# Performance work log

Measured on AMD Instinct MI355X. Metric: run time of the kernel, lower is better.

Reference implementation:

```python
import jax, jax.numpy as jnp
import numpy as np

SEQ_LEN, INPUT_DIM, HIDDEN_DIM, OUTPUT_DIM = 1024, 128, 256, 128
BATCH = 256


def setup_inputs() -> dict:
    key = jax.random.key(0)
    ks = jax.random.split(key, 7)
    s_ih = 1.0 / np.sqrt(INPUT_DIM)
    s_hh = 1.0 / np.sqrt(HIDDEN_DIM)
    return {
        "x": jax.random.normal(ks[0], (BATCH, SEQ_LEN, INPUT_DIM), jnp.float32),
        "W_ih": jax.random.normal(ks[1], (INPUT_DIM, 4 * HIDDEN_DIM), jnp.float32) * s_ih,
        "W_hh": jax.random.normal(ks[2], (HIDDEN_DIM, 4 * HIDDEN_DIM), jnp.float32) * s_hh,
        "b_ih": jax.random.normal(ks[3], (4 * HIDDEN_DIM,), jnp.float32) * s_hh,
        "b_hh": jax.random.normal(ks[4], (4 * HIDDEN_DIM,), jnp.float32) * s_hh,
        "W_out": jax.random.normal(ks[5], (HIDDEN_DIM, OUTPUT_DIM), jnp.float32) * s_hh,
        "b_out": jax.random.normal(ks[6], (OUTPUT_DIM,), jnp.float32) * s_hh,
    }


def reference(x, W_ih, W_hh, b_ih, b_hh, W_out, b_out):
    B, T, _ = x.shape
    H = W_hh.shape[0]
    # Precompute input projections for all timesteps: [T, B, 4H]
    x_proj = jnp.einsum("bti,ig->tbg", x, W_ih) + (b_ih + b_hh)

    def step(carry, xp_t):
        h, c = carry
        gates = xp_t + h @ W_hh  # [B, 4H]
        i_t, f_t, g_t, o_t = jnp.split(gates, 4, axis=1)
        i_t = jax.nn.sigmoid(i_t)
        f_t = jax.nn.sigmoid(f_t)
        g_t = jnp.tanh(g_t)
        o_t = jax.nn.sigmoid(o_t)
        c = f_t * c + i_t * g_t
        h = o_t * jnp.tanh(c)
        return (h, c), None

    h0 = jnp.zeros((B, H), x.dtype)
    c0 = jnp.zeros((B, H), x.dtype)
    (h_T, _), _ = jax.lax.scan(step, (h0, c0), x_proj)
    return h_T @ W_out + b_out
```

## Files before the change

### kernel.cpp

```cpp
#include <hip/hip_runtime.h>
#include <cstdint>


#define T_    1024
#define I_    128
#define H_    256

typedef short s8v __attribute__((ext_vector_type(8)));
typedef float f4v __attribute__((ext_vector_type(4)));
typedef unsigned short u16;
typedef unsigned int   u32;
typedef unsigned long long u64;

__device__ __forceinline__ u16 f2bf(float f) {
  union { float f; u32 u; } v; v.f = f;
  u32 r = v.u + 0x7FFFu + ((v.u >> 16) & 1u);
  return (u16)(r >> 16);
}
__device__ __forceinline__ float bf2f(u16 h) {
  union { u32 u; float f; } v; v.u = ((u32)h) << 16;
  return v.f;
}
__device__ __forceinline__ float sig_(float x)  { return 1.0f / (1.0f + __expf(-x)); }
__device__ __forceinline__ float tanh_(float x) { return 2.0f / (1.0f + __expf(-2.0f * x)) - 1.0f; }

__device__ __forceinline__ void unpack8(const u64 w[4], s8v& hi, s8v& lo) {
  #pragma unroll
  for (int j = 0; j < 4; j++) {
    u32 a = (u32)w[j], b = (u32)(w[j] >> 32);
    hi[2*j]   = (short)(u16)a;        lo[2*j]   = (short)(u16)(a >> 16);
    hi[2*j+1] = (short)(u16)b;        lo[2*j+1] = (short)(u16)(b >> 16);
  }
}

__global__ __launch_bounds__(256, 1) void lstm_persist(
    const float* __restrict__ x, const float* __restrict__ Wih,
    const float* __restrict__ Whh, const float* __restrict__ bih,
    const float* __restrict__ bhh, const float* __restrict__ Wout,
    const float* __restrict__ bout, float* __restrict__ out,
    u32* __restrict__ flags, u32* __restrict__ hbuf)
{
  const int bid  = blockIdx.x;
  const int xcd  = bid & 7;
  const int slot = bid >> 3;
  const int ct   = slot & 15;
  const int g    = ((slot >> 4) << 3) | xcd;
  const int tid  = threadIdx.x;
  const int wave = tid >> 6;
  const int lane = tid & 63;
  const int lm   = lane & 15;
  const int lq   = lane >> 4;

  __shared__ u16   Wlds[2][64][392];
  __shared__ u16   xlds[2][2][16][136];
  __shared__ float partial[4][4][16][20];

  for (int it = tid; it < 384 * 64; it += 256) {
    int k = it >> 6;
    int c = it & 63;
    int gcol = (c >> 4) * 256 + ct * 16 + (c & 15);
    float w = (k < 128) ? Wih[k * 1024 + gcol] : Whh[(k - 128) * 1024 + gcol];
    u16 hi = f2bf(w);
    Wlds[0][c][k] = hi;
    Wlds[1][c][k] = f2bf(w - bf2f(hi));
  }
  __syncthreads();

  s8v wfrag[3][4][2];
  #pragma unroll
  for (int ki = 0; ki < 3; ki++) {
    const int kt = wave + 4 * ki;
    #pragma unroll
    for (int gg = 0; gg < 4; gg++) {
      #pragma unroll
      for (int p = 0; p < 2; p++)
        wfrag[ki][gg][p] = *(const s8v*)&Wlds[p][gg * 16 + lm][kt * 32 + lq * 8];
    }
  }
  __syncthreads();

  const int cm  = tid >> 4;
  const int chc = tid & 15;
  float biasv[4];
  #pragma unroll
  for (int gg = 0; gg < 4; gg++) {
    int col = gg * 256 + ct * 16 + chc;
    biasv[gg] = bih[col] + bhh[col];
  }
  float cstate = 0.0f;

  const int xr  = tid >> 4;
  const int xc0 = (tid & 15) * 8;
  const float* xbase = x + (size_t)(g * 16 + xr) * (T_ * I_) + xc0;

  u32* gflags = flags + g * 32;
  const size_t hpar   = (size_t)16 * 16 * 256;
  const size_t hgbase = (size_t)g * 16 * 256;

  const int pl   = lane & 3;
  u32* fpeer = gflags + (2 * wave + (pl & 1) + 8 * (pl >> 1));

  auto xstore = [&](int par, float4 a, float4 b) {
    float v[8] = {a.x, a.y, a.z, a.w, b.x, b.y, b.z, b.w};
    union { u16 u[8]; s8v s; } hi, lo;
    #pragma unroll
    for (int j = 0; j < 8; j++) {
      u16 h = f2bf(v[j]);
      hi.u[j] = h;
      lo.u[j] = f2bf(v[j] - bf2f(h));
    }
    *(s8v*)&xlds[par][0][xr][xc0] = hi.s;
    *(s8v*)&xlds[par][1][xr][xc0] = lo.s;
  };

  {
    float4 a = *(const float4*)(xbase + 0);
    float4 b = *(const float4*)(xbase + 4);
    xstore(0, a, b);
  }
  __syncthreads();

  for (int t = 0; t < T_; t++) {
    const int par = t & 1;
    const int pn  = (t + 1) & 1;

    const int tn = (t + 1 < T_) ? (t + 1) : t;
    float4 xa = *(const float4*)(xbase + (size_t)tn * I_);
    float4 xb = *(const float4*)(xbase + (size_t)tn * I_ + 4);

    f4v acc[4];
    #pragma unroll
    for (int gg = 0; gg < 4; gg++)
      #pragma unroll
      for (int r = 0; r < 4; r++) acc[gg][r] = 0.0f;

    {
      s8v axh = *(const s8v*)&xlds[par][0][lm][wave * 32 + lq * 8];
      s8v axl = *(const s8v*)&xlds[par][1][lm][wave * 32 + lq * 8];
      #pragma unroll
      for (int gg = 0; gg < 4; gg++) {
        acc[gg] = __builtin_amdgcn_mfma_f32_16x16x32_bf16(axh, wfrag[0][gg][0], acc[gg], 0, 0, 0);
        acc[gg] = __builtin_amdgcn_mfma_f32_16x16x32_bf16(axl, wfrag[0][gg][0], acc[gg], 0, 0, 0);
        acc[gg] = __builtin_amdgcn_mfma_f32_16x16x32_bf16(axh, wfrag[0][gg][1], acc[gg], 0, 0, 0);
      }
    }

    if (t > 0) {
      const u32 s = (u32)t;
      while (true) {
        u32 f = __hip_atomic_load(fpeer, __ATOMIC_RELAXED, __HIP_MEMORY_SCOPE_AGENT);
        if (__all((int)((f - s) <= 1u))) break;
        __builtin_amdgcn_s_sleep(1);
      }
      asm volatile("" ::: "memory");

      const u32* hb0 = hbuf + (size_t)par * hpar + hgbase;
      #pragma unroll
      for (int ki = 1; ki < 3; ki++) {
        const int hk = wave * 32 + (ki - 1) * 128 + lq * 8;
        const u64* hp = (const u64*)(hb0 + (size_t)lm * 256 + hk);
        u64 w[4];
        #pragma unroll
        for (int j = 0; j < 4; j++)
          w[j] = __hip_atomic_load(hp + j, __ATOMIC_RELAXED, __HIP_MEMORY_SCOPE_AGENT);
        s8v ahh, ahl;
        unpack8(w, ahh, ahl);
        #pragma unroll
        for (int gg = 0; gg < 4; gg++) {
          acc[gg] = __builtin_amdgcn_mfma_f32_16x16x32_bf16(ahh, wfrag[ki][gg][0], acc[gg], 0, 0, 0);
          acc[gg] = __builtin_amdgcn_mfma_f32_16x16x32_bf16(ahl, wfrag[ki][gg][0], acc[gg], 0, 0, 0);
          acc[gg] = __builtin_amdgcn_mfma_f32_16x16x32_bf16(ahh, wfrag[ki][gg][1], acc[gg], 0, 0, 0);
        }
      }
    }

    #pragma unroll
    for (int gg = 0; gg < 4; gg++)
      #pragma unroll
      for (int r = 0; r < 4; r++)
        partial[wave][gg][lq * 4 + r][lm] = acc[gg][r];
    __syncthreads();

    float ga = biasv[0], gb = biasv[1], gc = biasv[2], gd = biasv[3];
    #pragma unroll
    for (int w = 0; w < 4; w++) {
      ga += partial[w][0][cm][chc];
      gb += partial[w][1][cm][chc];
      gc += partial[w][2][cm][chc];
      gd += partial[w][3][cm][chc];
    }
    float i_t = sig_(ga), f_t = sig_(gb), g_t = tanh_(gc), o_t = sig_(gd);
    cstate = f_t * cstate + i_t * g_t;
    float h = o_t * tanh_(cstate);

    u16 hhi = f2bf(h);
    u16 hlo = f2bf(h - bf2f(hhi));
    u32 pk  = ((u32)hlo << 16) | (u32)hhi;
    u32* hw = hbuf + (size_t)pn * hpar + hgbase + (size_t)cm * 256 + ct * 16 + chc;
    __hip_atomic_store(hw, pk, __ATOMIC_RELAXED, __HIP_MEMORY_SCOPE_AGENT);

    __syncthreads();
    if (tid == 0)
      __hip_atomic_store(gflags + ct, (u32)(t + 1), __ATOMIC_RELAXED, __HIP_MEMORY_SCOPE_AGENT);

    xstore(pn, xa, xb);
    __syncthreads();
  }

  {
    const u32 s = (u32)T_;
    u32* fp = gflags + lm;
    while (true) {
      u32 f = __hip_atomic_load(fp, __ATOMIC_RELAXED, __HIP_MEMORY_SCOPE_AGENT);
      if (__all((int)((f - s) <= 1u))) break;
      __builtin_amdgcn_s_sleep(1);
    }
    asm volatile("" ::: "memory");
  }
  __syncthreads();
  for (int it = tid; it < 16 * 256; it += 256) {
    int n = it >> 8;
    int k = it & 255;
    float w = (n < 8) ? Wout[k * 128 + ct * 8 + n] : 0.0f;
    u16 hi = f2bf(w);
    Wlds[0][n][k] = hi;
    Wlds[1][n][k] = f2bf(w - bf2f(hi));
  }
  __syncthreads();

  f4v oacc;
  #pragma unroll
  for (int r = 0; r < 4; r++) oacc[r] = 0.0f;
  const u32* hb0 = hbuf + hgbase;
  #pragma unroll
  for (int ki = 0; ki < 2; ki++) {
    const int hk = (wave * 2 + ki) * 32 + lq * 8;
    const u64* hp = (const u64*)(hb0 + (size_t)lm * 256 + hk);
    u64 w[4];
    #pragma unroll
    for (int j = 0; j < 4; j++)
      w[j] = __hip_atomic_load(hp + j, __ATOMIC_RELAXED, __HIP_MEMORY_SCOPE_AGENT);
    s8v ahh, ahl;
    unpack8(w, ahh, ahl);
    s8v bh  = *(const s8v*)&Wlds[0][lm][hk];
    s8v bl  = *(const s8v*)&Wlds[1][lm][hk];
    oacc = __builtin_amdgcn_mfma_f32_16x16x32_bf16(ahh, bh, oacc, 0, 0, 0);
    oacc = __builtin_amdgcn_mfma_f32_16x16x32_bf16(ahl, bh, oacc, 0, 0, 0);
    oacc = __builtin_amdgcn_mfma_f32_16x16x32_bf16(ahh, bl, oacc, 0, 0, 0);
  }
  #pragma unroll
  for (int r = 0; r < 4; r++) partial[wave][0][lq * 4 + r][lm] = oacc[r];
  __syncthreads();

  if (tid < 128) {
    int m  = tid >> 3;
    int oc = tid & 7;
    float v = bout[ct * 8 + oc];
    #pragma unroll
    for (int w = 0; w < 4; w++) v += partial[w][0][m][oc];
    out[(size_t)(g * 16 + m) * 128 + ct * 8 + oc] = v;
  }
}

extern "C" void kernel_launch(void* const* d_in, const int* in_sizes, int n_in,
                              void* d_out, int out_size, void* d_ws, size_t ws_size,
                              hipStream_t stream) {
  const float* x    = (const float*)d_in[0];
  const float* Wih  = (const float*)d_in[1];
  const float* Whh  = (const float*)d_in[2];
  const float* bih  = (const float*)d_in[3];
  const float* bhh  = (const float*)d_in[4];
  const float* Wout = (const float*)d_in[5];
  const float* bout = (const float*)d_in[6];
  float* out = (float*)d_out;

  char* ws = (char*)d_ws;
  u32* flags = (u32*)ws;
  u32* hbuf  = (u32*)(ws + 4096);

  hipLaunchKernelGGL(lstm_persist, dim3(256), dim3(256), 0, stream,
                     x, Wih, Whh, bih, bhh, Wout, bout, out, flags, hbuf);
}
```

Baseline: 3.131 ms.

## Replace flag-based step sync with tagged hidden-state polling in LSTM persistent kernel

Drops the per-block step flags and instead stores a 2-bit step tag in the low bits of the bf16 residual of each published hidden value, so consumers poll the hidden-state data itself until every tag matches. This removes a flag store and a second barrier per step, and folds the flag wait and the data load into a single round trip. The next-step x staging is moved before the first barrier, and the end-of-step barrier only waits on LDS counters. The cost is a slightly truncated low-order hidden residual, plus reliance on per-word atomicity and initialisation of the tags in the buffer.

```diff
diff --git a/kernel.cpp b/kernel.cpp
--- a/kernel.cpp
+++ b/kernel.cpp
@@ -31,6 +31,18 @@
     hi[2*j]   = (short)(u16)a;        lo[2*j]   = (short)(u16)(a >> 16);
     hi[2*j+1] = (short)(u16)b;        lo[2*j+1] = (short)(u16)(b >> 16);
   }
+}
+
+__device__ __forceinline__ bool tagok(u64 w, u32 tag) {
+  return ((((u32)(w >> 16)) & 3u) == tag) & ((((u32)(w >> 48)) & 3u) == tag);
+}
+
+__device__ __forceinline__ void lgkm_barrier() {
+  asm volatile("s_waitcnt lgkmcnt(0)" ::: "memory");
+  __builtin_amdgcn_sched_barrier(0);
+  __builtin_amdgcn_s_barrier();
+  __builtin_amdgcn_sched_barrier(0);
+  asm volatile("" ::: "memory");
 }
 
 __global__ __launch_bounds__(256, 1) void lstm_persist(
@@ -40,6 +52,7 @@
     const float* __restrict__ bout, float* __restrict__ out,
     u32* __restrict__ flags, u32* __restrict__ hbuf)
 {
+  (void)flags;
   const int bid  = blockIdx.x;
   const int xcd  = bid & 7;
   const int slot = bid >> 3;
@@ -55,6 +68,18 @@
   __shared__ u16   xlds[2][2][16][136];
   __shared__ float partial[4][4][16][20];
 
+  const int cm  = tid >> 4;
+  const int chc = tid & 15;
+
+  const size_t hpar   = (size_t)16 * 16 * 256;
+  const size_t hgbase = (size_t)g * 16 * 256;
+
+  {
+    u32* hz = hbuf + hgbase + (size_t)cm * 256 + ct * 16 + chc;
+    __hip_atomic_store(hz,        0x00010000u, __ATOMIC_RELAXED, __HIP_MEMORY_SCOPE_AGENT);
+    __hip_atomic_store(hz + hpar, 0u,          __ATOMIC_RELAXED, __HIP_MEMORY_SCOPE_AGENT);
+  }
+
   for (int it = tid; it < 384 * 64; it += 256) {
     int k = it >> 6;
     int c = it & 63;
@@ -79,8 +104,6 @@
   }
   __syncthreads();
 
-  const int cm  = tid >> 4;
-  const int chc = tid & 15;
   float biasv[4];
   #pragma unroll
   for (int gg = 0; gg < 4; gg++) {
@@ -92,13 +115,6 @@
   const int xr  = tid >> 4;
   const int xc0 = (tid & 15) * 8;
   const float* xbase = x + (size_t)(g * 16 + xr) * (T_ * I_) + xc0;
-
-  u32* gflags = flags + g * 32;
-  const size_t hpar   = (size_t)16 * 16 * 256;
-  const size_t hgbase = (size_t)g * 16 * 256;
-
-  const int pl   = lane & 3;
-  u32* fpeer = gflags + (2 * wave + (pl & 1) + 8 * (pl >> 1));
 
   auto xstore = [&](int par, float4 a, float4 b) {
     float v[8] = {a.x, a.y, a.z, a.w, b.x, b.y, b.z, b.w};
@@ -146,30 +162,41 @@
     }
 
     if (t > 0) {
-      const u32 s = (u32)t;
+      const u32 tag = (u32)(t & 3);
+      const u32* hb0 = hbuf + (size_t)par * hpar + hgbase;
+      const u64* hp1 = (const u64*)(hb0 + (size_t)lm * 256 + (wave * 32 + lq * 8));
+      const u64* hp2 = (const u64*)(hb0 + (size_t)lm * 256 + (wave * 32 + 128 + lq * 8));
+      u64 w1[4], w2[4];
       while (true) {
-        u32 f = __hip_atomic_load(fpeer, __ATOMIC_RELAXED, __HIP_MEMORY_SCOPE_AGENT);
-        if (__all((int)((f - s) <= 1u))) break;
+        #pragma unroll
+        for (int j = 0; j < 4; j++) {
+          w1[j] = __hip_atomic_load(hp1 + j, __ATOMIC_RELAXED, __HIP_MEMORY_SCOPE_AGENT);
+          w2[j] = __hip_atomic_load(hp2 + j, __ATOMIC_RELAXED, __HIP_MEMORY_SCOPE_AGENT);
+        }
+        bool ok = true;
+        #pragma unroll
+        for (int j = 0; j < 4; j++) {
+          ok &= tagok(w1[j], tag);
+          ok &= tagok(w2[j], tag);
+        }
+        if (__all(ok)) break;
         __builtin_amdgcn_s_sleep(1);
       }
-      asm volatile("" ::: "memory");
-
-      const u32* hb0 = hbuf + (size_t)par * hpar + hgbase;
-      #pragma unroll
-      for (int ki = 1; ki < 3; ki++) {
-        const int hk = wave * 32 + (ki - 1) * 128 + lq * 8;
-        const u64* hp = (const u64*)(hb0 + (size_t)lm * 256 + hk);
-        u64 w[4];
-        #pragma unroll
-        for (int j = 0; j < 4; j++)
-          w[j] = __hip_atomic_load(hp + j, __ATOMIC_RELAXED, __HIP_MEMORY_SCOPE_AGENT);
+      {
         s8v ahh, ahl;
-        unpack8(w, ahh, ahl);
+        unpack8(w1, ahh, ahl);
         #pragma unroll
         for (int gg = 0; gg < 4; gg++) {
-          acc[gg] = __builtin_amdgcn_mfma_f32_16x16x32_bf16(ahh, wfrag[ki][gg][0], acc[gg], 0, 0, 0);
-          acc[gg] = __builtin_amdgcn_mfma_f32_16x16x32_bf16(ahl, wfrag[ki][gg][0], acc[gg], 0, 0, 0);
-          acc[gg] = __builtin_amdgcn_mfma_f32_16x16x32_bf16(ahh, wfrag[ki][gg][1], acc[gg], 0, 0, 0);
+          acc[gg] = __builtin_amdgcn_mfma_f32_16x16x32_bf16(ahh, wfrag[1][gg][0], acc[gg], 0, 0, 0);
+          acc[gg] = __builtin_amdgcn_mfma_f32_16x16x32_bf16(ahl, wfrag[1][gg][0], acc[gg], 0, 0, 0);
+          acc[gg] = __builtin_amdgcn_mfma_f32_16x16x32_bf16(ahh, wfrag[1][gg][1], acc[gg], 0, 0, 0);
+        }
+        unpack8(w2, ahh, ahl);
+        #pragma unroll
+        for (int gg = 0; gg < 4; gg++) {
+          acc[gg] = __builtin_amdgcn_mfma_f32_16x16x32_bf16(ahh, wfrag[2][gg][0], acc[gg], 0, 0, 0);
+          acc[gg] = __builtin_amdgcn_mfma_f32_16x16x32_bf16(ahl, wfrag[2][gg][0], acc[gg], 0, 0, 0);
+          acc[gg] = __builtin_amdgcn_mfma_f32_16x16x32_bf16(ahh, wfrag[2][gg][1], acc[gg], 0, 0, 0);
         }
       }
     }
@@ -179,6 +206,9 @@
       #pragma unroll
       for (int r = 0; r < 4; r++)
         partial[wave][gg][lq * 4 + r][lm] = acc[gg][r];
+
+    xstore(pn, xa, xb);
+
     __syncthreads();
 
     float ga = biasv[0], gb = biasv[1], gc = biasv[2], gd = biasv[3];
@@ -195,27 +225,33 @@
 
     u16 hhi = f2bf(h);
     u16 hlo = f2bf(h - bf2f(hhi));
-    u32 pk  = ((u32)hlo << 16) | (u32)hhi;
+    u32 pk  = ((u32)((hlo & 0xFFFCu) | (u32)((t + 1) & 3)) << 16) | (u32)hhi;
     u32* hw = hbuf + (size_t)pn * hpar + hgbase + (size_t)cm * 256 + ct * 16 + chc;
     __hip_atomic_store(hw, pk, __ATOMIC_RELAXED, __HIP_MEMORY_SCOPE_AGENT);
 
-    __syncthreads();
-    if (tid == 0)
-      __hip_atomic_store(gflags + ct, (u32)(t + 1), __ATOMIC_RELAXED, __HIP_MEMORY_SCOPE_AGENT);
-
-    xstore(pn, xa, xb);
-    __syncthreads();
-  }
-
+    lgkm_barrier();
+  }
+
+  u64 wf0[4], wf1[4];
   {
-    const u32 s = (u32)T_;
-    u32* fp = gflags + lm;
+    const u32* hb0 = hbuf + hgbase;
+    const u64* hpa = (const u64*)(hb0 + (size_t)lm * 256 + ((wave * 2 + 0) * 32 + lq * 8));
+    const u64* hpb = (const u64*)(hb0 + (size_t)lm * 256 + ((wave * 2 + 1) * 32 + lq * 8));
     while (true) {
-      u32 f = __hip_atomic_load(fp, __ATOMIC_RELAXED, __HIP_MEMORY_SCOPE_AGENT);
-      if (__all((int)((f - s) <= 1u))) break;
+      #pragma unroll
+      for (int j = 0; j < 4; j++) {
+        wf0[j] = __hip_atomic_load(hpa + j, __ATOMIC_RELAXED, __HIP_MEMORY_SCOPE_AGENT);
+        wf1[j] = __hip_atomic_load(hpb + j, __ATOMIC_RELAXED, __HIP_MEMORY_SCOPE_AGENT);
+      }
+      bool ok = true;
+      #pragma unroll
+      for (int j = 0; j < 4; j++) {
+        ok &= tagok(wf0[j], 0u);
+        ok &= tagok(wf1[j], 0u);
+      }
+      if (__all(ok)) break;
       __builtin_amdgcn_s_sleep(1);
     }
-    asm volatile("" ::: "memory");
   }
   __syncthreads();
   for (int it = tid; it < 16 * 256; it += 256) {
@@ -231,17 +267,11 @@
   f4v oacc;
   #pragma unroll
   for (int r = 0; r < 4; r++) oacc[r] = 0.0f;
-  const u32* hb0 = hbuf + hgbase;
   #pragma unroll
   for (int ki = 0; ki < 2; ki++) {
     const int hk = (wave * 2 + ki) * 32 + lq * 8;
-    const u64* hp = (const u64*)(hb0 + (size_t)lm * 256 + hk);
-    u64 w[4];
-    #pragma unroll
-    for (int j = 0; j < 4; j++)
-      w[j] = __hip_atomic_load(hp + j, __ATOMIC_RELAXED, __HIP_MEMORY_SCOPE_AGENT);
     s8v ahh, ahl;
-    unpack8(w, ahh, ahl);
+    unpack8(ki == 0 ? wf0 : wf1, ahh, ahl);
     s8v bh  = *(const s8v*)&Wlds[0][lm][hk];
     s8v bl  = *(const s8v*)&Wlds[1][lm][hk];
     oacc = __builtin_amdgcn_mfma_f32_16x16x32_bf16(ahh, bh, oacc, 0, 0, 0);
@@ -277,7 +307,6 @@
   char* ws = (char*)d_ws;
   u32* flags = (u32*)ws;
   u32* hbuf  = (u32*)(ws + 4096);
-
   hipLaunchKernelGGL(lstm_persist, dim3(256), dim3(256), 0, stream,
                      x, Wih, Whh, bih, bhh, Wout, bout, out, flags, hbuf);
 }
```

New measurement: 3.260 ms. +4.1%, slower.
